# Optimization experiments

Hardware: AMD Instinct MI355X
Metric: run time of the kernel (lower is better)

Reference implementation:

```python
import jax, jax.numpy as jnp
import numpy as np


def _ln(x, w, b):
    m = jnp.mean(x, axis=-1, keepdims=True)
    v = jnp.var(x, axis=-1, keepdims=True)
    return (x - m) / jnp.sqrt(v + 1e-5) * w + b


def setup_inputs() -> dict:
    B, T, C = 4, 2048, 1024
    E_RWKV, E = 2, 3          # 2 RWKV experts + 1 transformer expert
    H = 4 * C                 # RWKV FFN hidden
    S = 0.02                  # init scale
    key = jax.random.key(0)
    ks = jax.random.split(key, 20)
    d = {}
    d["x"] = jax.random.normal(ks[0], (B, T, C), jnp.float32)
    d["v_first"] = jax.random.normal(ks[1], (B, T, C), jnp.float32)
    d["capital_shares"] = jax.random.uniform(ks[2], (E,), jnp.float32)
    # layer norms
    d["ln1_w"] = jnp.ones((C,), jnp.float32)
    d["ln1_b"] = jnp.zeros((C,), jnp.float32)
    d["ln2_w"] = jnp.ones((C,), jnp.float32)
    d["ln2_b"] = jnp.zeros((C,), jnp.float32)
    # simplified RWKV time-mix (gated linear attention stand-in)
    d["Wr"] = S * jax.random.normal(ks[3], (C, C), jnp.float32)
    d["Wv"] = S * jax.random.normal(ks[4], (C, C), jnp.float32)
    d["Wo"] = S * jax.random.normal(ks[5], (C, C), jnp.float32)
    d["Ws"] = S * jax.random.normal(ks[6], (C, C), jnp.float32)
    # RWKV FFN experts (squared-ReLU channel mix)
    d["K_rwkv"] = S * jax.random.normal(ks[7], (E_RWKV, C, H), jnp.float32)
    d["V_rwkv"] = S * jax.random.normal(ks[8], (E_RWKV, H, C), jnp.float32)
    d["conf_rwkv"] = S * jax.random.normal(ks[9], (E_RWKV, C), jnp.float32)
    # transformer expert (state-gated)
    d["W1"] = S * jax.random.normal(ks[10], (C, C), jnp.float32)
    d["W2"] = S * jax.random.normal(ks[11], (C, C), jnp.float32)
    d["W3"] = S * jax.random.normal(ks[12], (C, C), jnp.float32)
    d["conf_trans"] = S * jax.random.normal(ks[13], (C,), jnp.float32)
    # critic
    d["w_diff"] = S * jax.random.normal(ks[14], (C,), jnp.float32)
    d["W_aff"] = S * jax.random.normal(ks[15], (C, E), jnp.float32)
    # bridge (h -> rwkv_state reconstruction)
    d["W_bridge"] = S * jax.random.normal(ks[16], (C, C), jnp.float32)
    return d


def reference(x, v_first, capital_shares, ln1_w, ln1_b, ln2_w, ln2_b,
              Wr, Wv, Wo, Ws, K_rwkv, V_rwkv, conf_rwkv,
              W1, W2, W3, conf_trans, w_diff, W_aff, W_bridge):
    B, T, C = x.shape
    # attention (simplified time-mix): gated linear projection + state head
    xln = _ln(x, ln1_w, ln1_b)
    att_out = (jax.nn.sigmoid(xln @ Wr) * (xln @ Wv)) @ Wo
    rwkv_state = xln @ Ws
    x = x + att_out
    h = _ln(x, ln2_w, ln2_b)

    # per-expert confidences  (B, T, E)
    conf_r = jax.nn.sigmoid(jnp.einsum('btc,ec->bte', h, conf_rwkv))
    conf_t = jax.nn.sigmoid(h @ conf_trans)[..., None]
    confidences = jnp.concatenate([conf_r, conf_t], axis=-1)
    E = confidences.shape[-1]

    # critic + market routing: bids = conf * capital * difficulty + affinity subsidy
    difficulty = jax.nn.sigmoid(h @ w_diff)[..., None]          # (B, T, 1)
    affinity = h @ W_aff                                         # (B, T, E)
    bids = confidences * capital_shares * difficulty + affinity
    winners = jnp.argmax(bids, axis=-1)                          # (B, T) int

    flat_h = h.reshape(-1, C)                # (N, C)
    flat_state = rwkv_state.reshape(-1, C)   # (N, C)
    flat_w = winners.reshape(-1)             # (N,)
    flat_conf = confidences.reshape(-1, E)

    # straight-through confidence scale: conf / (stop_grad(conf) + eps)
    win_conf = jnp.take_along_axis(flat_conf, flat_w[:, None], axis=1)  # (N, 1)
    scale = win_conf / (jax.lax.stop_gradient(win_conf) + 1e-6)

    # expert compute (dense-per-expert, combined by winner mask -> same math
    # as gather/scatter dispatch in the torch loop)
    hr = jnp.square(jax.nn.relu(jnp.einsum('nc,ech->enh', flat_h, K_rwkv)))
    out_rwkv = jnp.einsum('enh,ehc->enc', hr, V_rwkv)            # (E_rwkv, N, C)
    out_trans = ((flat_h @ W1) * jax.nn.sigmoid(flat_state @ W2)) @ W3
    all_out = jnp.concatenate([out_rwkv, out_trans[None]], axis=0)  # (E, N, C)

    onehot = jax.nn.one_hot(flat_w, E, dtype=flat_h.dtype)       # (N, E)
    final = jnp.einsum('ne,enc->nc', onehot, all_out) * scale    # (N, C)
    return x + final.reshape(B, T, C)
```

## Files before the change

kernel.cpp:

```cpp
#include <hip/hip_runtime.h>
#include <stdint.h>


#define N_TOK 8192
#define C_DIM 1024
#define H_DIM 4096

typedef unsigned short u16;
typedef __attribute__((ext_vector_type(8))) short short8;
typedef _Float16 half8 __attribute__((ext_vector_type(8)));
typedef __attribute__((ext_vector_type(4))) float floatx4;

__device__ __forceinline__ float b2f(u16 u) {
  union { unsigned u; float f; } v; v.u = ((unsigned)u) << 16; return v.f;
}
__device__ __forceinline__ u16 f2b(float f) {
  union { float f; unsigned u; } v; v.f = f;
  unsigned r = v.u + 0x7fffu + ((v.u >> 16) & 1u);
  return (u16)(r >> 16);
}
__device__ __forceinline__ u16 f2h(float f) {
  union { _Float16 h; u16 u; } v; v.h = (_Float16)f; return v.u;
}
__device__ __forceinline__ float sigf(float x) { return 1.f / (1.f + __expf(-x)); }

typedef __attribute__((address_space(3))) unsigned int lds_uint;
typedef const __attribute__((address_space(1))) unsigned int glob_uint;
__device__ __forceinline__ void gld16(u16* lds, const u16* g) {
  __builtin_amdgcn_global_load_lds((glob_uint*)g, (lds_uint*)lds, 16, 0, 0);
}
__device__ __forceinline__ floatx4 mf(short8 a, short8 b, floatx4 c) {
  return __builtin_amdgcn_mfma_f32_16x16x32_bf16(a, b, c, 0, 0, 0);
}
__device__ __forceinline__ floatx4 mfh(half8 a, half8 b, floatx4 c) {
  return __builtin_amdgcn_mfma_f32_16x16x32_f16(a, b, c, 0, 0, 0);
}
__device__ __forceinline__ int3 swzr(int nx, int ny, int ntot) {
  const int lin = ((int)blockIdx.z * ny + (int)blockIdx.y) * nx + (int)blockIdx.x;
  const int xcd = lin & 7, s = lin >> 3;
  const int row = (s / nx) * 8 + xcd;
  int3 r;
  r.x = s % nx;
  r.y = row % ny;
  r.z = row / ny;
  return r;
}
__device__ __forceinline__ void stage2(u16* s, const u16* g, int K, int base,
                                       int c0, int c1, int k0) {
  gld16(s + c0 * 8, g + (size_t)(base + (c0 >> 2)) * K + k0 + (c0 & 3) * 8);
  gld16(s + c1 * 8, g + (size_t)(base + (c1 >> 2)) * K + k0 + (c1 & 3) * 8);
}
__device__ __forceinline__ void stage1(u16* s, const u16* g, int K, int base,
                                       int c, int k0) {
  gld16(s + c * 8, g + (size_t)(base + (c >> 2)) * K + k0 + (c & 3) * 8);
}
template <typename V>
__device__ __forceinline__ void fragN(V* f, const u16* s, int wo, int fr, int fk, int n) {
  for (int i = 0; i < n; i++) f[i] = *(const V*)(s + (wo + i * 16 + fr) * 32 + fk);
}

__global__ __launch_bounds__(256) void gemm_rv(
    const u16* __restrict__ Ahi, const u16* __restrict__ Alo,
    const u16* __restrict__ Brh, const u16* __restrict__ Brl,
    const u16* __restrict__ Bvh, const u16* __restrict__ Bvl,
    int K, int NC, u16* __restrict__ Ghi, u16* __restrict__ Glo,
    u16* __restrict__ G16) {
  __shared__ __align__(16) u16 sAh[4096], sAl[4096];
  __shared__ __align__(16) u16 sRh[2048], sRl[2048], sVh[2048], sVl[2048];
  const int3 b = swzr(16, 64, 1024);
  const int tid = threadIdx.x, lane = tid & 63, wave = tid >> 6;
  const int rowbase = b.y * 128, colbase = b.x * 64;
  const int wm = (wave >> 1) * 64, wn = (wave & 1) * 32;
  floatx4 ar[4][2] = {}, av[4][2] = {};
  const int c0 = tid, c1 = tid + 256;
  for (int k0 = 0; k0 < K; k0 += 32) {
    __syncthreads();
    stage2(sAh, Ahi, K, rowbase, c0, c1, k0);
    stage2(sAl, Alo, K, rowbase, c0, c1, k0);
    stage1(sRh, Brh, K, colbase, c0, k0);
    stage1(sRl, Brl, K, colbase, c0, k0);
    stage1(sVh, Bvh, K, colbase, c0, k0);
    stage1(sVl, Bvl, K, colbase, c0, k0);
    __syncthreads();
    const int fr = lane & 15, fk = (lane >> 4) * 8;
    short8 ah[4], al[4], rh[2], rl[2], vh[2], vl[2];
    fragN(ah, sAh, wm, fr, fk, 4); fragN(al, sAl, wm, fr, fk, 4);
    fragN(rh, sRh, wn, fr, fk, 2); fragN(rl, sRl, wn, fr, fk, 2);
    fragN(vh, sVh, wn, fr, fk, 2); fragN(vl, sVl, wn, fr, fk, 2);
#pragma unroll
    for (int mi = 0; mi < 4; mi++)
#pragma unroll
      for (int ni = 0; ni < 2; ni++) {
        ar[mi][ni] = mf(ah[mi], rh[ni], ar[mi][ni]);
        ar[mi][ni] = mf(ah[mi], rl[ni], ar[mi][ni]);
        ar[mi][ni] = mf(al[mi], rh[ni], ar[mi][ni]);
        av[mi][ni] = mf(ah[mi], vh[ni], av[mi][ni]);
        av[mi][ni] = mf(ah[mi], vl[ni], av[mi][ni]);
        av[mi][ni] = mf(al[mi], vh[ni], av[mi][ni]);
      }
  }
  const int col0 = lane & 15, row0 = (lane >> 4) * 4;
#pragma unroll
  for (int mi = 0; mi < 4; mi++)
#pragma unroll
    for (int ni = 0; ni < 2; ni++)
#pragma unroll
      for (int r = 0; r < 4; r++) {
        const int row = rowbase + wm + mi * 16 + row0 + r;
        const int col = colbase + wn + ni * 16 + col0;
        const size_t idx = (size_t)row * NC + col;
        const float g = sigf(ar[mi][ni][r]) * av[mi][ni][r];
        const u16 h = f2b(g);
        Ghi[idx] = h;
        Glo[idx] = f2b(g - b2f(h));
        G16[idx] = f2h(g);
      }
}

__global__ __launch_bounds__(256) void gemm_wo_f16(
    const u16* __restrict__ A, const u16* __restrict__ BT, int K, int NC,
    const float* __restrict__ Xin, float* __restrict__ Xnew) {
  __shared__ __align__(16) u16 sA0[4096], sA1[4096], sB0[2048], sB1[2048];
  const int3 b = swzr(16, 64, 1024);
  const int tid = threadIdx.x, lane = tid & 63, wave = tid >> 6;
  const int rowbase = b.y * 128, colbase = b.x * 64;
  const int wm = (wave >> 1) * 64, wn = (wave & 1) * 32;
  floatx4 acc[4][2] = {};
  const int c0 = tid, c1 = tid + 256;
  for (int k0 = 0; k0 < K; k0 += 64) {
    __syncthreads();
    stage2(sA0, A, K, rowbase, c0, c1, k0);
    stage2(sA1, A, K, rowbase, c0, c1, k0 + 32);
    stage1(sB0, BT, K, colbase, c0, k0);
    stage1(sB1, BT, K, colbase, c0, k0 + 32);
    __syncthreads();
    const int fr = lane & 15, fk = (lane >> 4) * 8;
    half8 af[4], bf[2];
    fragN(af, sA0, wm, fr, fk, 4);
    fragN(bf, sB0, wn, fr, fk, 2);
#pragma unroll
    for (int mi = 0; mi < 4; mi++)
#pragma unroll
      for (int ni = 0; ni < 2; ni++)
        acc[mi][ni] = mfh(af[mi], bf[ni], acc[mi][ni]);
    fragN(af, sA1, wm, fr, fk, 4);
    fragN(bf, sB1, wn, fr, fk, 2);
#pragma unroll
    for (int mi = 0; mi < 4; mi++)
#pragma unroll
      for (int ni = 0; ni < 2; ni++)
        acc[mi][ni] = mfh(af[mi], bf[ni], acc[mi][ni]);
  }
  const int col0 = lane & 15, row0 = (lane >> 4) * 4;
#pragma unroll
  for (int mi = 0; mi < 4; mi++)
#pragma unroll
    for (int ni = 0; ni < 2; ni++)
#pragma unroll
      for (int r = 0; r < 4; r++) {
        const int row = rowbase + wm + mi * 16 + row0 + r;
        const int col = colbase + wn + ni * 16 + col0;
        const size_t idx = (size_t)row * NC + col;
        Xnew[idx] = Xin[idx] + acc[mi][ni][r];
      }
}

__global__ __launch_bounds__(256) void expert_mid(
    const u16* __restrict__ hb, const u16* __restrict__ xlnh,
    const int* __restrict__ idx,
    const u16* __restrict__ KT0p, const u16* __restrict__ KT1p,
    const u16* __restrict__ W1T, const u16* __restrict__ MTp,
    const int* __restrict__ counts, int base,
    u16* __restrict__ hr0, u16* __restrict__ hr1, u16* __restrict__ tg) {
  __shared__ __align__(16) u16 smem[12288];
  const int3 b = swzr(32, 32, 3072);
  const int z = b.z;
  const int tid = threadIdx.x, lane = tid & 63, wave = tid >> 6;
  const int rowbase = b.y * 128;
  const int c0 = tid, c1 = tid + 256;
  const int fr = lane & 15, fk = (lane >> 4) * 8;
  const int col0 = lane & 15, row00 = (lane >> 4) * 4;
  if (z < 2) {
    const int cnt = counts[z] - base;
    if (rowbase >= cnt) return;
    const u16* BT = z ? KT1p : KT0p;
    const int* idxA = idx + z * N_TOK + base;
    u16* Cout = z ? hr1 : hr0;
    u16* sA = smem;
    u16* sB = smem + 4096;
    const int colbase = b.x * 128;
    const int wm = (wave >> 1) * 64, wn = (wave & 1) * 64;
    floatx4 acc[4][4] = {};
    const int g0 = idxA[rowbase + (c0 >> 2)], g1 = idxA[rowbase + (c1 >> 2)];
    const u16* pA0 = hb + (size_t)g0 * C_DIM + (c0 & 3) * 8;
    const u16* pA1 = hb + (size_t)g1 * C_DIM + (c1 & 3) * 8;
    const u16* pB0 = BT + (size_t)(colbase + (c0 >> 2)) * C_DIM + (c0 & 3) * 8;
    const u16* pB1 = BT + (size_t)(colbase + (c1 >> 2)) * C_DIM + (c1 & 3) * 8;
    for (int k0 = 0; k0 < C_DIM; k0 += 32) {
      __syncthreads();
      gld16(sA + c0 * 8, pA0 + k0);
      gld16(sA + c1 * 8, pA1 + k0);
      gld16(sB + c0 * 8, pB0 + k0);
      gld16(sB + c1 * 8, pB1 + k0);
      __syncthreads();
      short8 af[4], bf[4];
      fragN(af, sA, wm, fr, fk, 4);
      fragN(bf, sB, wn, fr, fk, 4);
#pragma unroll
      for (int mi = 0; mi < 4; mi++)
#pragma unroll
        for (int ni = 0; ni < 4; ni++)
          acc[mi][ni] = mf(af[mi], bf[ni], acc[mi][ni]);
    }
#pragma unroll
    for (int mi = 0; mi < 4; mi++)
#pragma unroll
      for (int ni = 0; ni < 4; ni++)
#pragma unroll
        for (int r = 0; r < 4; r++) {
          const int row = rowbase + wm + mi * 16 + row00 + r;
          const int col = colbase + wn + ni * 16 + col0;
          const float v = acc[mi][ni][r];
          const float t = v > 0.f ? v * v : 0.f;
          Cout[(size_t)row * H_DIM + col] = f2b(t);
        }
  } else {
    if (b.x >= 16) return;
    const int cnt = counts[2] - base;
    if (rowbase >= cnt) return;
    const int* idxA = idx + 2 * N_TOK + base;
    u16* s1 = smem;
    u16* s2 = smem + 4096;
    u16* sB1 = smem + 8192;
    u16* sB2 = smem + 10240;
    const int colbase = b.x * 64;
    const int wm = (wave >> 1) * 64, wn = (wave & 1) * 32;
    floatx4 a1[4][2] = {}, a2[4][2] = {};
    const int g0 = idxA[rowbase + (c0 >> 2)], g1 = idxA[rowbase + (c1 >> 2)];
    const u16* p10 = hb + (size_t)g0 * C_DIM + (c0 & 3) * 8;
    const u16* p11 = hb + (size_t)g1 * C_DIM + (c1 & 3) * 8;
    const u16* p20 = xlnh + (size_t)g0 * C_DIM + (c0 & 3) * 8;
    const u16* p21 = xlnh + (size_t)g1 * C_DIM + (c1 & 3) * 8;
    for (int k0 = 0; k0 < C_DIM; k0 += 32) {
      __syncthreads();
      gld16(s1 + c0 * 8, p10 + k0);
      gld16(s1 + c1 * 8, p11 + k0);
      gld16(s2 + c0 * 8, p20 + k0);
      gld16(s2 + c1 * 8, p21 + k0);
      stage1(sB1, W1T, C_DIM, colbase, c0, k0);
      stage1(sB2, MTp, C_DIM, colbase, c0, k0);
      __syncthreads();
      short8 f1[4], f2[4], b1[2], b2[2];
      fragN(f1, s1, wm, fr, fk, 4); fragN(f2, s2, wm, fr, fk, 4);
      fragN(b1, sB1, wn, fr, fk, 2); fragN(b2, sB2, wn, fr, fk, 2);
#pragma unroll
      for (int mi = 0; mi < 4; mi++)
#pragma unroll
        for (int ni = 0; ni < 2; ni++) {
          a1[mi][ni] = mf(f1[mi], b1[ni], a1[mi][ni]);
          a2[mi][ni] = mf(f2[mi], b2[ni], a2[mi][ni]);
        }
    }
#pragma unroll
    for (int mi = 0; mi < 4; mi++)
#pragma unroll
      for (int ni = 0; ni < 2; ni++)
#pragma unroll
        for (int r = 0; r < 4; r++) {
          const int row = rowbase + wm + mi * 16 + row00 + r;
          const int col = colbase + wn + ni * 16 + col0;
          tg[(size_t)(base + row) * C_DIM + col] =
              f2b(a1[mi][ni][r] * sigf(a2[mi][ni][r]));
        }
  }
}

__global__ __launch_bounds__(256) void vgemm3(
    const u16* __restrict__ hr0, const u16* __restrict__ hr1,
    const u16* __restrict__ tg,
    const u16* __restrict__ VT0p, const u16* __restrict__ VT1p,
    const u16* __restrict__ W3T,
    const int* __restrict__ counts, int base, const int* __restrict__ idx,
    const float* __restrict__ x_new, const float* __restrict__ scalep,
    float* __restrict__ out) {
  const int3 b = swzr(8, 32, 768);
  const int z = b.z;
  const int cnt = counts[z] - base;
  const int rowbase = b.y * 128;
  if (rowbase >= cnt) return;
  const u16* A; const u16* BT; int K; int arow;
  if (z == 0)      { A = hr0; BT = VT0p; K = H_DIM; arow = rowbase; }
  else if (z == 1) { A = hr1; BT = VT1p; K = H_DIM; arow = rowbase; }
  else             { A = tg;  BT = W3T;  K = C_DIM; arow = base + rowbase; }
  const int* idxO = idx + z * N_TOK + base;
  __shared__ __align__(16) u16 sA0[4096], sA1[4096], sB0[4096], sB1[4096];
  const int tid = threadIdx.x, lane = tid & 63, wave = tid >> 6;
  const int colbase = b.x * 128;
  const int wm = (wave >> 1) * 64, wn = (wave & 1) * 64;
  floatx4 acc[4][4] = {};
  const int c0 = tid, c1 = tid + 256;
  for (int k0 = 0; k0 < K; k0 += 64) {
    __syncthreads();
    stage2(sA0, A, K, arow, c0, c1, k0);
    stage2(sA1, A, K, arow, c0, c1, k0 + 32);
    stage2(sB0, BT, K, colbase, c0, c1, k0);
    stage2(sB1, BT, K, colbase, c0, c1, k0 + 32);
    __syncthreads();
    const int fr = lane & 15, fk = (lane >> 4) * 8;
    short8 af[4], bf[4];
    fragN(af, sA0, wm, fr, fk, 4);
    fragN(bf, sB0, wn, fr, fk, 4);
#pragma unroll
    for (int mi = 0; mi < 4; mi++)
#pragma unroll
      for (int ni = 0; ni < 4; ni++)
        acc[mi][ni] = mf(af[mi], bf[ni], acc[mi][ni]);
    fragN(af, sA1, wm, fr, fk, 4);
    fragN(bf, sB1, wn, fr, fk, 4);
#pragma unroll
    for (int mi = 0; mi < 4; mi++)
#pragma unroll
      for (int ni = 0; ni < 4; ni++)
        acc[mi][ni] = mf(af[mi], bf[ni], acc[mi][ni]);
  }
  const int col0 = lane & 15, row0 = (lane >> 4) * 4;
#pragma unroll
  for (int mi = 0; mi < 4; mi++)
#pragma unroll
    for (int ni = 0; ni < 4; ni++)
#pragma unroll
      for (int r = 0; r < 4; r++) {
        const int row = rowbase + wm + mi * 16 + row0 + r;
        if (row < cnt) {
          const int col = colbase + wn + ni * 16 + col0;
          const int g = idxO[row];
          const size_t o = (size_t)g * C_DIM + col;
          out[o] = x_new[o] + acc[mi][ni][r] * scalep[g];
        }
      }
}

template <int EPI>
__global__ __launch_bounds__(256) void ggemm(
    const u16* __restrict__ A, const int* __restrict__ idxA,
    const u16* __restrict__ BT, int K, int NC,
    const int* __restrict__ cntp, int base,
    u16* __restrict__ Cout,
    const float* __restrict__ x_new, const float* __restrict__ scalep,
    const int* __restrict__ idxO, float* __restrict__ out) {
  const int cnt = cntp ? (*cntp - base) : (int)(gridDim.y * 128);
  if ((int)blockIdx.y * 128 >= cnt) return;
  __shared__ __align__(16) u16 sA[4096], sB[4096];
  const int tid = threadIdx.x, lane = tid & 63, wave = tid >> 6;
  const int rowbase = blockIdx.y * 128, colbase = blockIdx.x * 128;
  const int wm = (wave >> 1) * 64, wn = (wave & 1) * 64;
  floatx4 acc[4][4] = {};
  const int c0 = tid, c1 = tid + 256;
  const int r0 = rowbase + (c0 >> 2), r1 = rowbase + (c1 >> 2);
  const int g0 = idxA ? idxA[base + r0] : r0;
  const int g1 = idxA ? idxA[base + r1] : r1;
  const u16* pA0 = A + (size_t)g0 * K + (c0 & 3) * 8;
  const u16* pA1 = A + (size_t)g1 * K + (c1 & 3) * 8;
  const u16* pB0 = BT + (size_t)(colbase + (c0 >> 2)) * K + (c0 & 3) * 8;
  const u16* pB1 = BT + (size_t)(colbase + (c1 >> 2)) * K + (c1 & 3) * 8;
  for (int k0 = 0; k0 < K; k0 += 32) {
    __syncthreads();
    gld16(sA + c0 * 8, pA0 + k0);
    gld16(sA + c1 * 8, pA1 + k0);
    gld16(sB + c0 * 8, pB0 + k0);
    gld16(sB + c1 * 8, pB1 + k0);
    __syncthreads();
    const int fr = lane & 15, fk = (lane >> 4) * 8;
    short8 af[4], bf[4];
    fragN(af, sA, wm, fr, fk, 4);
    fragN(bf, sB, wn, fr, fk, 4);
#pragma unroll
    for (int mi = 0; mi < 4; mi++)
#pragma unroll
      for (int ni = 0; ni < 4; ni++)
        acc[mi][ni] = mf(af[mi], bf[ni], acc[mi][ni]);
  }
  const int col0 = lane & 15, row00 = (lane >> 4) * 4;
#pragma unroll
  for (int mi = 0; mi < 4; mi++)
#pragma unroll
    for (int ni = 0; ni < 4; ni++)
#pragma unroll
      for (int r = 0; r < 4; r++) {
        const int row = rowbase + wm + mi * 16 + row00 + r;
        const int col = colbase + wn + ni * 16 + col0;
        const float v = acc[mi][ni][r];
        if constexpr (EPI == 0) {
          Cout[(size_t)row * NC + col] = f2b(v);
        } else if constexpr (EPI == 2) {
          const float t = v > 0.f ? v * v : 0.f;
          Cout[(size_t)row * NC + col] = f2b(t);
        } else {
          if (row < cnt) {
            const int g = idxO[base + row];
            const size_t o = (size_t)g * NC + col;
            out[o] = x_new[o] + v * scalep[g];
          }
        }
      }
}

struct CCBatchArgs {
  const float *Wr, *Wv, *Wo, *W1, *W2, *W3;
  u16 *WrTh, *WrTl, *WvTh, *WvTl, *WoT16, *W1T, *W2T, *W3T;
};
__global__ __launch_bounds__(256) void transpose_cc_batch(CCBatchArgs a) {
  __shared__ float tile[32][33];
  const int z = blockIdx.z;
  const float* in; u16* oh; u16* ol = nullptr; int mode;
  switch (z) {
    case 0: in = a.Wr; oh = a.WrTh; ol = a.WrTl; mode = 1; break;
    case 1: in = a.Wv; oh = a.WvTh; ol = a.WvTl; mode = 1; break;
    case 2: in = a.Wo; oh = a.WoT16; mode = 2; break;
    case 3: in = a.W1; oh = a.W1T; mode = 0; break;
    case 4: in = a.W2; oh = a.W2T; mode = 0; break;
    default: in = a.W3; oh = a.W3T; mode = 0; break;
  }
  const int tx = threadIdx.x & 31, ty = threadIdx.x >> 5;
  const int bx = blockIdx.x * 32, by = blockIdx.y * 32;
#pragma unroll
  for (int i = 0; i < 32; i += 8)
    tile[ty + i][tx] = in[(size_t)(by + ty + i) * C_DIM + bx + tx];
  __syncthreads();
#pragma unroll
  for (int i = 0; i < 32; i += 8) {
    const float v = tile[tx][ty + i];
    const size_t o = (size_t)(bx + ty + i) * C_DIM + by + tx;
    if (mode == 2) {
      oh[o] = f2h(v);
    } else {
      const u16 h = f2b(v);
      oh[o] = h;
      if (mode == 1) ol[o] = f2b(v - b2f(h));
    }
  }
}

__global__ __launch_bounds__(256) void transpose_kv(
    const float* __restrict__ in, u16* __restrict__ o0, u16* __restrict__ o1,
    int R, int Cc) {
  __shared__ float tile[32][33];
  const float* ip = in + (size_t)blockIdx.z * R * Cc;
  u16* oh = blockIdx.z ? o1 : o0;
  const int tx = threadIdx.x & 31, ty = threadIdx.x >> 5;
  const int bx = blockIdx.x * 32, by = blockIdx.y * 32;
#pragma unroll
  for (int i = 0; i < 32; i += 8)
    tile[ty + i][tx] = ip[(size_t)(by + ty + i) * Cc + bx + tx];
  __syncthreads();
#pragma unroll
  for (int i = 0; i < 32; i += 8)
    oh[(size_t)(bx + ty + i) * R + by + tx] = f2b(tile[tx][ty + i]);
}

__global__ __launch_bounds__(256) void cast_kernel(const float* __restrict__ in,
                                                   u16* __restrict__ o, int n) {
  const int i = blockIdx.x * 256 + threadIdx.x;
  if (i < n) o[i] = f2b(in[i]);
}

__global__ __launch_bounds__(256) void ln_kernel(
    const float* __restrict__ x, const float* __restrict__ w,
    const float* __restrict__ b, u16* __restrict__ oh, u16* __restrict__ ol) {
  const int row = blockIdx.x, tid = threadIdx.x;
  const float* xr = x + (size_t)row * C_DIM;
  float vals[4], s = 0.f, ss = 0.f;
#pragma unroll
  for (int i = 0; i < 4; i++) {
    const float t = xr[tid + i * 256];
    vals[i] = t; s += t; ss += t * t;
  }
  for (int off = 32; off; off >>= 1) {
    s += __shfl_xor(s, off, 64);
    ss += __shfl_xor(ss, off, 64);
  }
  __shared__ float red[8];
  const int lane = tid & 63, wave = tid >> 6;
  if (lane == 0) { red[wave] = s; red[4 + wave] = ss; }
  __syncthreads();
  const float S = red[0] + red[1] + red[2] + red[3];
  const float SS = red[4] + red[5] + red[6] + red[7];
  const float mean = S * (1.f / C_DIM);
  const float var = SS * (1.f / C_DIM) - mean * mean;
  const float inv = rsqrtf(var + 1e-5f);
#pragma unroll
  for (int i = 0; i < 4; i++) {
    const int c = tid + i * 256;
    const float y = (vals[i] - mean) * inv * w[c] + b[c];
    const u16 h = f2b(y);
    oh[(size_t)row * C_DIM + c] = h;
    ol[(size_t)row * C_DIM + c] = f2b(y - b2f(h));
  }
}

__global__ __launch_bounds__(256) void prep_vec(
    const float* __restrict__ ln2w, const float* __restrict__ ln2b,
    const float* __restrict__ conf_rwkv, const float* __restrict__ conf_trans,
    const float* __restrict__ w_diff, const float* __restrict__ W_aff,
    float* __restrict__ p, float* __restrict__ sg, float* __restrict__ sb) {
  const int j = blockIdx.x, tid = threadIdx.x;
  float gs = 0.f, bs = 0.f;
#pragma unroll
  for (int i = 0; i < 4; i++) {
    const int c = tid + i * 256;
    float wv;
    if (j == 0) wv = conf_rwkv[c];
    else if (j == 1) wv = conf_rwkv[C_DIM + c];
    else if (j == 2) wv = conf_trans[c];
    else if (j == 3) wv = w_diff[c];
    else wv = W_aff[c * 3 + (j - 4)];
    const float pv = ln2w[c] * wv;
    p[j * C_DIM + c] = pv;
    gs += pv;
    bs += ln2b[c] * wv;
  }
  for (int off = 32; off; off >>= 1) {
    gs += __shfl_xor(gs, off, 64);
    bs += __shfl_xor(bs, off, 64);
  }
  __shared__ float red[8];
  const int lane = tid & 63, wave = tid >> 6;
  if (lane == 0) { red[wave] = gs; red[4 + wave] = bs; }
  __syncthreads();
  if (tid == 0) {
    sg[j] = red[0] + red[1] + red[2] + red[3];
    sb[j] = red[4] + red[5] + red[6] + red[7];
  }
}

__global__ __launch_bounds__(256) void ugemv(
    const float* __restrict__ Wo, const float* __restrict__ p,
    float* __restrict__ u) {
  const int o = blockIdx.x * 4 + (threadIdx.x >> 6);
  const int lane = threadIdx.x & 63;
  const int j = o >> 10, k = o & 1023;
  float s = 0.f;
#pragma unroll
  for (int i = 0; i < 16; i++) {
    const int c = lane + i * 64;
    s += Wo[(size_t)k * C_DIM + c] * p[j * C_DIM + c];
  }
  for (int off = 32; off; off >>= 1) s += __shfl_xor(s, off, 64);
  if (lane == 0) u[o] = s;
}

__global__ __launch_bounds__(256) void route_kernel(
    const float* __restrict__ x, const float* __restrict__ xn,
    const u16* __restrict__ ghi, const u16* __restrict__ glo,
    const float* __restrict__ p, const float* __restrict__ u,
    const float* __restrict__ sg, const float* __restrict__ sb,
    const float* __restrict__ ln2w, const float* __restrict__ ln2b,
    const float* __restrict__ capital,
    int* __restrict__ winner, float* __restrict__ scale, u16* __restrict__ oh,
    int* __restrict__ pz, int nz) {
  {
    const int i = blockIdx.x * 256 + threadIdx.x;
    if (i < nz) pz[i] = 0;
  }
  const int token = blockIdx.x * 4 + (threadIdx.x >> 6);
  const int lane = threadIdx.x & 63;
  const float* xnr = xn + (size_t)token * C_DIM;
  float xv[16], s = 0.f, ss = 0.f;
#pragma unroll
  for (int i = 0; i < 16; i++) {
    const float t = xnr[lane + i * 64];
    xv[i] = t; s += t; ss += t * t;
  }
  for (int off = 32; off; off >>= 1) {
    s += __shfl_xor(s, off, 64);
    ss += __shfl_xor(ss, off, 64);
  }
  const float mean = s * (1.f / C_DIM);
  const float var = ss * (1.f / C_DIM) - mean * mean;
  const float inv = rsqrtf(var + 1e-5f);
  float acc[7] = {};
#pragma unroll
  for (int i = 0; i < 16; i++) {
    const int c = lane + i * 64;
    oh[(size_t)token * C_DIM + c] = f2b((xv[i] - mean) * inv * ln2w[c] + ln2b[c]);
    const float xc = x[(size_t)token * C_DIM + c];
    const float gc = b2f(ghi[(size_t)token * C_DIM + c]) +
                     b2f(glo[(size_t)token * C_DIM + c]);
#pragma unroll
    for (int j = 0; j < 7; j++)
      acc[j] += xc * p[j * C_DIM + c] + gc * u[j * C_DIM + c];
  }
  for (int off = 32; off; off >>= 1)
#pragma unroll
    for (int j = 0; j < 7; j++) acc[j] += __shfl_xor(acc[j], off, 64);
  if (lane == 0) {
    float hw[7];
#pragma unroll
    for (int j = 0; j < 7; j++) hw[j] = acc[j] * inv - mean * inv * sg[j] + sb[j];
    const float conf[3] = {1.f / (1.f + expf(-hw[0])), 1.f / (1.f + expf(-hw[1])),
                           1.f / (1.f + expf(-hw[2]))};
    const float diff = 1.f / (1.f + expf(-hw[3]));
    int best = 0; float bb = -1e30f;
#pragma unroll
    for (int e = 0; e < 3; e++) {
      const float bid = conf[e] * capital[e] * diff + hw[4 + e];
      if (bid > bb) { bb = bid; best = e; }
    }
    winner[token] = best;
    scale[token] = conf[best] / (conf[best] + 1e-6f);
  }
}

__global__ __launch_bounds__(256) void compact_kernel(
    const int* __restrict__ winner, int* __restrict__ idx, int* __restrict__ counts) {
  const int t = blockIdx.x * 256 + threadIdx.x;
  const int w = winner[t];
  const int pos = atomicAdd(counts + w, 1);
  idx[w * N_TOK + pos] = t;
}

extern "C" void kernel_launch(void* const* d_in, const int* in_sizes, int n_in,
                              void* d_out, int out_size, void* d_ws, size_t ws_size,
                              hipStream_t stream) {
  const float* x = (const float*)d_in[0];
  const float* capital = (const float*)d_in[2];
  const float* ln1w = (const float*)d_in[3];
  const float* ln1b = (const float*)d_in[4];
  const float* ln2w = (const float*)d_in[5];
  const float* ln2b = (const float*)d_in[6];
  const float* Wr = (const float*)d_in[7];
  const float* Wv = (const float*)d_in[8];
  const float* Wo = (const float*)d_in[9];
  const float* Wsm = (const float*)d_in[10];
  const float* Krwkv = (const float*)d_in[11];
  const float* Vrwkv = (const float*)d_in[12];
  const float* conf_rwkv = (const float*)d_in[13];
  const float* W1 = (const float*)d_in[14];
  const float* W2 = (const float*)d_in[15];
  const float* W3 = (const float*)d_in[16];
  const float* conf_trans = (const float*)d_in[17];
  const float* w_diff = (const float*)d_in[18];
  const float* W_aff = (const float*)d_in[19];
  float* out = (float*)d_out;

  char* ws = (char*)d_ws;
  size_t off = 0;
  auto alloc = [&](size_t bytes) -> char* {
    char* pp = ws + off;
    off += (bytes + 255) & ~(size_t)255;
    return pp;
  };
  const size_t CC = (size_t)C_DIM * C_DIM * 2;
  const size_t CH = (size_t)C_DIM * H_DIM * 2;
  const size_t NCb = (size_t)N_TOK * C_DIM * 2;
  u16* WrTh = (u16*)alloc(CC); u16* WrTl = (u16*)alloc(CC);
  u16* WvTh = (u16*)alloc(CC); u16* WvTl = (u16*)alloc(CC);
  u16* WoT16 = (u16*)alloc(CC);
  u16* W1T = (u16*)alloc(CC);
  u16* W2T = (u16*)alloc(CC);
  u16* W3T = (u16*)alloc(CC);
  u16* Wsb = (u16*)alloc(CC);
  u16* MT  = (u16*)alloc(CC);
  u16* KT0 = (u16*)alloc(CH);
  u16* VT0 = (u16*)alloc(CH);
  u16* KT1 = (u16*)alloc(CH);
  u16* VT1 = (u16*)alloc(CH);
  u16* xlnh = (u16*)alloc(NCb);
  u16* xlnl = (u16*)alloc(NCb);
  u16* ghi = (u16*)alloc(NCb);
  u16* glo = (u16*)alloc(NCb);
  u16* g16 = (u16*)alloc(NCb);
  float* x_new = (float*)alloc((size_t)N_TOK * C_DIM * 4);
  u16* hr1 = (u16*)alloc((size_t)4096 * H_DIM * 2);
  u16* hr0 = glo;
  int* idx = (int*)alloc(3 * N_TOK * 4);
  int* counts = (int*)alloc(256);
  int* winner = (int*)alloc(N_TOK * 4);
  float* scalep = (float*)alloc(N_TOK * 4);
  float* pvec = (float*)alloc(7 * C_DIM * 4);
  float* uvec = (float*)alloc(7 * C_DIM * 4);
  float* sgv = (float*)alloc(256);
  float* sbv = (float*)alloc(256);

  const dim3 blk(256);
  CCBatchArgs ta = {Wr, Wv, Wo, W1, W2, W3,
                    WrTh, WrTl, WvTh, WvTl, WoT16, W1T, W2T, W3T};
  transpose_cc_batch<<<dim3(32, 32, 6), blk, 0, stream>>>(ta);
  transpose_kv<<<dim3(H_DIM / 32, C_DIM / 32, 2), blk, 0, stream>>>(
      Krwkv, KT0, KT1, C_DIM, H_DIM);
  transpose_kv<<<dim3(C_DIM / 32, H_DIM / 32, 2), blk, 0, stream>>>(
      Vrwkv, VT0, VT1, H_DIM, C_DIM);
  cast_kernel<<<(C_DIM * C_DIM) / 256, blk, 0, stream>>>(Wsm, Wsb, C_DIM * C_DIM);
  ggemm<0><<<dim3(8, 8), blk, 0, stream>>>(W2T, nullptr, Wsb, C_DIM, C_DIM,
      nullptr, 0, MT, nullptr, nullptr, nullptr, nullptr);
  prep_vec<<<7, blk, 0, stream>>>(ln2w, ln2b, conf_rwkv, conf_trans, w_diff,
                                  W_aff, pvec, sgv, sbv);
  ugemv<<<7 * C_DIM / 4, blk, 0, stream>>>(Wo, pvec, uvec);

  ln_kernel<<<N_TOK, blk, 0, stream>>>(x, ln1w, ln1b, xlnh, xlnl);

  gemm_rv<<<dim3(C_DIM / 64, N_TOK / 128), blk, 0, stream>>>(
      xlnh, xlnl, WrTh, WrTl, WvTh, WvTl, C_DIM, C_DIM, ghi, glo, g16);
  gemm_wo_f16<<<dim3(C_DIM / 64, N_TOK / 128), blk, 0, stream>>>(
      g16, WoT16, C_DIM, C_DIM, x, x_new);
  u16* hb = xlnl;
  route_kernel<<<N_TOK / 4, blk, 0, stream>>>(x, x_new, ghi, glo, pvec, uvec,
      sgv, sbv, ln2w, ln2b, capital, winner, scalep, hb, idx, 3 * N_TOK + 64);
  compact_kernel<<<N_TOK / 256, blk, 0, stream>>>(winner, idx, counts);

  u16* tg = ghi;
  for (int c = 0; c < 2; c++) {
    const int base = c * 4096;
    expert_mid<<<dim3(H_DIM / 128, 32, 3), blk, 0, stream>>>(
        hb, xlnh, idx, KT0, KT1, W1T, MT, counts, base, hr0, hr1, tg);
    vgemm3<<<dim3(8, 32, 3), blk, 0, stream>>>(
        hr0, hr1, tg, VT0, VT1, W3T, counts, base, idx, x_new, scalep, out);
  }
}
```

Baseline: 696.9 us.

## Double-buffer shared-memory staging in expert_mid and vgemm3 GEMM loops

Converts the K-loops of the expert up-projection (z<2 path) and the down-projection kernel into double-buffered pipelines. The next K tile is issued into the alternate LDS buffer before the MFMAs on the current tile, and each iteration now needs one barrier instead of two. The aim is to overlap global-to-LDS loads with matrix math and cut synchronisation stalls. In exchange, LDS use doubles (32KB and 64KB per block), which may reduce occupancy. It also relies on gld16/stage2 completing before the single barrier.

```diff
diff --git a/kernel.cpp b/kernel.cpp
--- a/kernel.cpp
+++ b/kernel.cpp
@@ -172,7 +172,7 @@
     const u16* __restrict__ W1T, const u16* __restrict__ MTp,
     const int* __restrict__ counts, int base,
     u16* __restrict__ hr0, u16* __restrict__ hr1, u16* __restrict__ tg) {
-  __shared__ __align__(16) u16 smem[12288];
+  __shared__ __align__(16) u16 smem[16384];
   const int3 b = swzr(32, 32, 3072);
   const int z = b.z;
   const int tid = threadIdx.x, lane = tid & 63, wave = tid >> 6;
@@ -186,8 +186,6 @@
     const u16* BT = z ? KT1p : KT0p;
     const int* idxA = idx + z * N_TOK + base;
     u16* Cout = z ? hr1 : hr0;
-    u16* sA = smem;
-    u16* sB = smem + 4096;
     const int colbase = b.x * 128;
     const int wm = (wave >> 1) * 64, wn = (wave & 1) * 64;
     floatx4 acc[4][4] = {};
@@ -196,13 +194,24 @@
     const u16* pA1 = hb + (size_t)g1 * C_DIM + (c1 & 3) * 8;
     const u16* pB0 = BT + (size_t)(colbase + (c0 >> 2)) * C_DIM + (c0 & 3) * 8;
     const u16* pB1 = BT + (size_t)(colbase + (c1 >> 2)) * C_DIM + (c1 & 3) * 8;
+    gld16(smem + c0 * 8, pA0);
+    gld16(smem + c1 * 8, pA1);
+    gld16(smem + 4096 + c0 * 8, pB0);
+    gld16(smem + 4096 + c1 * 8, pB1);
+    __syncthreads();
+    int cur = 0;
     for (int k0 = 0; k0 < C_DIM; k0 += 32) {
-      __syncthreads();
-      gld16(sA + c0 * 8, pA0 + k0);
-      gld16(sA + c1 * 8, pA1 + k0);
-      gld16(sB + c0 * 8, pB0 + k0);
-      gld16(sB + c1 * 8, pB1 + k0);
-      __syncthreads();
+      const int nxt = cur ^ 1;
+      if (k0 + 32 < C_DIM) {
+        u16* dA = smem + nxt * 8192;
+        u16* dB = dA + 4096;
+        gld16(dA + c0 * 8, pA0 + k0 + 32);
+        gld16(dA + c1 * 8, pA1 + k0 + 32);
+        gld16(dB + c0 * 8, pB0 + k0 + 32);
+        gld16(dB + c1 * 8, pB1 + k0 + 32);
+      }
+      const u16* sA = smem + cur * 8192;
+      const u16* sB = sA + 4096;
       short8 af[4], bf[4];
       fragN(af, sA, wm, fr, fk, 4);
       fragN(bf, sB, wn, fr, fk, 4);
@@ -211,6 +220,8 @@
 #pragma unroll
         for (int ni = 0; ni < 4; ni++)
           acc[mi][ni] = mf(af[mi], bf[ni], acc[mi][ni]);
+      __syncthreads();
+      cur = nxt;
     }
 #pragma unroll
     for (int mi = 0; mi < 4; mi++)
@@ -293,35 +304,49 @@
   else if (z == 1) { A = hr1; BT = VT1p; K = H_DIM; arow = rowbase; }
   else             { A = tg;  BT = W3T;  K = C_DIM; arow = base + rowbase; }
   const int* idxO = idx + z * N_TOK + base;
-  __shared__ __align__(16) u16 sA0[4096], sA1[4096], sB0[4096], sB1[4096];
+  __shared__ __align__(16) u16 smem[32768];
   const int tid = threadIdx.x, lane = tid & 63, wave = tid >> 6;
   const int colbase = b.x * 128;
   const int wm = (wave >> 1) * 64, wn = (wave & 1) * 64;
   floatx4 acc[4][4] = {};
   const int c0 = tid, c1 = tid + 256;
+  {
+    u16* d = smem;
+    stage2(d, A, K, arow, c0, c1, 0);
+    stage2(d + 4096, A, K, arow, c0, c1, 32);
+    stage2(d + 8192, BT, K, colbase, c0, c1, 0);
+    stage2(d + 12288, BT, K, colbase, c0, c1, 32);
+  }
+  __syncthreads();
+  int cur = 0;
   for (int k0 = 0; k0 < K; k0 += 64) {
-    __syncthreads();
-    stage2(sA0, A, K, arow, c0, c1, k0);
-    stage2(sA1, A, K, arow, c0, c1, k0 + 32);
-    stage2(sB0, BT, K, colbase, c0, c1, k0);
-    stage2(sB1, BT, K, colbase, c0, c1, k0 + 32);
-    __syncthreads();
+    const int nxt = cur ^ 1;
+    if (k0 + 64 < K) {
+      u16* d = smem + nxt * 16384;
+      stage2(d, A, K, arow, c0, c1, k0 + 64);
+      stage2(d + 4096, A, K, arow, c0, c1, k0 + 96);
+      stage2(d + 8192, BT, K, colbase, c0, c1, k0 + 64);
+      stage2(d + 12288, BT, K, colbase, c0, c1, k0 + 96);
+    }
+    const u16* s = smem + cur * 16384;
     const int fr = lane & 15, fk = (lane >> 4) * 8;
     short8 af[4], bf[4];
-    fragN(af, sA0, wm, fr, fk, 4);
-    fragN(bf, sB0, wn, fr, fk, 4);
+    fragN(af, s, wm, fr, fk, 4);
+    fragN(bf, s + 8192, wn, fr, fk, 4);
 #pragma unroll
     for (int mi = 0; mi < 4; mi++)
 #pragma unroll
       for (int ni = 0; ni < 4; ni++)
         acc[mi][ni] = mf(af[mi], bf[ni], acc[mi][ni]);
-    fragN(af, sA1, wm, fr, fk, 4);
-    fragN(bf, sB1, wn, fr, fk, 4);
+    fragN(af, s + 4096, wm, fr, fk, 4);
+    fragN(bf, s + 12288, wn, fr, fk, 4);
 #pragma unroll
     for (int mi = 0; mi < 4; mi++)
 #pragma unroll
       for (int ni = 0; ni < 4; ni++)
         acc[mi][ni] = mf(af[mi], bf[ni], acc[mi][ni]);
+    __syncthreads();
+    cur = nxt;
   }
   const int col0 = lane & 15, row0 = (lane >> 4) * 4;
 #pragma unroll
```

Result: slower. 727.3 us (+4.4%).
